# Kernel optimization log

Measured on AMD Instinct MI355X. Metric: run time of the kernel, lower is better.

## Reference

```python
import jax, jax.numpy as jnp
import numpy as np

N_NODES = 50000
N_EDGES = 800000
IN_CH = 128
OUT_CH = 32
HID = 2 * OUT_CH  # 64


def setup_inputs() -> dict:
    key = jax.random.key(0)
    ks = jax.random.split(key, 8)
    x = jax.random.normal(ks[0], (N_NODES, IN_CH), dtype=jnp.float32)
    edge_index = jax.random.randint(ks[1], (2, N_EDGES), 0, N_NODES, dtype=jnp.int32)
    s1 = 1.0 / np.sqrt(IN_CH)
    s2 = 1.0 / np.sqrt(HID)
    W1 = jax.random.normal(ks[2], (IN_CH, HID), dtype=jnp.float32) * s1
    b1 = jnp.zeros((HID,), dtype=jnp.float32)
    W_mu = jax.random.normal(ks[3], (HID, OUT_CH), dtype=jnp.float32) * s2
    b_mu = jnp.zeros((OUT_CH,), dtype=jnp.float32)
    W_logstd = jax.random.normal(ks[4], (HID, OUT_CH), dtype=jnp.float32) * s2
    b_logstd = jnp.zeros((OUT_CH,), dtype=jnp.float32)
    return {"x": x, "edge_index": edge_index, "W1": W1, "b1": b1,
            "W_mu": W_mu, "b_mu": b_mu, "W_logstd": W_logstd, "b_logstd": b_logstd}


def _gcn_norm(edge_index, n, dtype):
    # PyG GCNConv: add self-loops, symmetric normalization D^-1/2 A D^-1/2
    loops = jnp.arange(n, dtype=edge_index.dtype)
    src = jnp.concatenate([edge_index[0], loops])
    dst = jnp.concatenate([edge_index[1], loops])
    deg = jax.ops.segment_sum(jnp.ones_like(dst, dtype=dtype), dst, num_segments=n)
    deg_inv_sqrt = jnp.where(deg > 0, jax.lax.rsqrt(deg), 0.0)
    norm = deg_inv_sqrt[src] * deg_inv_sqrt[dst]  # [E+N]
    return src, dst, norm


def _gcn_conv(x, W, b, src, dst, norm, n):
    h = x @ W                        # transform first (in >= out)
    msg = h[src] * norm[:, None]     # gather + scale, [E+N, out]
    out = jax.ops.segment_sum(msg, dst, num_segments=n)
    return out + b


def reference(x, edge_index, W1, b1, W_mu, b_mu, W_logstd, b_logstd):
    n = x.shape[0]
    src, dst, norm = _gcn_norm(edge_index, n, x.dtype)
    h = jax.nn.relu(_gcn_conv(x, W1, b1, src, dst, norm, n))
    mu = _gcn_conv(h, W_mu, b_mu, src, dst, norm, n)
    logstd = _gcn_conv(h, W_logstd, b_logstd, src, dst, norm, n)
    return mu, logstd
```

## Files before the change

kernel.cpp:

```cpp
#include <hip/hip_runtime.h>
#include <hip/hip_fp16.h>

#define N_NODES 50000
#define N_EDGES 800000
#define IN_CH 128
#define HID 64
#define OUT_CH 32
#define CAP 64
#define ZROW N_NODES

union H4 { uint2 u; __half2 h[2]; };

__global__ __launch_bounds__(256) void k_scatter(const int* __restrict__ ei,
                                                 int* cur, int* __restrict__ pk,
                                                 unsigned* zA, unsigned* zB) {
    if (blockIdx.x == 0 && threadIdx.x < 32) { zA[threadIdx.x] = 0u; zB[threadIdx.x] = 0u; }
    int g = blockIdx.x * 256 + threadIdx.x;
    if (g >= N_EDGES / 2) return;
    int2 ss = ((const int2*)ei)[g];
    int2 dd = ((const int2*)(ei + N_EDGES))[g];
    int p0 = (dd.x << 6) + atomicAdd(&cur[dd.x], 1);
    pk[p0] = ss.x;
    int p1 = (dd.y << 6) + atomicAdd(&cur[dd.y], 1);
    pk[p1] = ss.y;
}

__global__ __launch_bounds__(256) void k_mm1(const float* __restrict__ x,
                                             const float* __restrict__ W1,
                                             const int* __restrict__ cur,
                                             __half* __restrict__ t1) {
    __shared__ float4 ws[64 * 16];
    __shared__ float  xsT[64 * 64];
    int t = threadIdx.x;
    int n0 = blockIdx.x * 64;
    int lane = t & 63, wv_ = t >> 6;
    int ni = lane >> 2;
    int cq = ((lane & 3) << 2) + wv_;
    const float4* W4 = (const float4*)W1;
    const float4* x4 = (const float4*)x;
    float4 acc0 = {0,0,0,0}, acc1 = acc0, acc2 = acc0, acc3 = acc0;
#pragma unroll
    for (int kt = 0; kt < 2; ++kt) {
        __syncthreads();
#pragma unroll
        for (int i = 0; i < 4; ++i) {
            int L = i * 256 + t;
            ws[L] = W4[kt * 1024 + L];
            int n = L >> 4, q = L & 15;
            int ng = n0 + n; if (ng >= N_NODES) ng = N_NODES - 1;
            float4 v = x4[ng * 32 + kt * 16 + q];
            int fb = q * 256 + (((n >> 2) ^ q) << 2) + (n & 3);
            xsT[fb]       = v.x;
            xsT[fb + 64]  = v.y;
            xsT[fb + 128] = v.z;
            xsT[fb + 192] = v.w;
        }
        __syncthreads();
        const float4* xsT4 = (const float4*)xsT;
#pragma unroll 8
        for (int k = 0; k < 64; ++k) {
            float4 xv = xsT4[k * 16 + (ni ^ (k >> 2))];
            float4 wvv = ws[k * 16 + cq];
            acc0.x += xv.x * wvv.x; acc0.y += xv.x * wvv.y; acc0.z += xv.x * wvv.z; acc0.w += xv.x * wvv.w;
            acc1.x += xv.y * wvv.x; acc1.y += xv.y * wvv.y; acc1.z += xv.y * wvv.z; acc1.w += xv.y * wvv.w;
            acc2.x += xv.z * wvv.x; acc2.y += xv.z * wvv.y; acc2.z += xv.z * wvv.z; acc2.w += xv.z * wvv.w;
            acc3.x += xv.w * wvv.x; acc3.y += xv.w * wvv.y; acc3.z += xv.w * wvv.z; acc3.w += xv.w * wvv.w;
        }
    }
    int nb = n0 + 4 * ni;
    if (nb < N_NODES) {
        int4 c4 = *(const int4*)(cur + nb);
        float d0 = rsqrtf((float)c4.x + 1.0f);
        float d1 = rsqrtf((float)c4.y + 1.0f);
        float d2 = rsqrtf((float)c4.z + 1.0f);
        float d3 = rsqrtf((float)c4.w + 1.0f);
        uint2* o2 = (uint2*)t1;
        H4 v;
        v.h[0] = __floats2half2_rn(d0 * acc0.x, d0 * acc0.y);
        v.h[1] = __floats2half2_rn(d0 * acc0.z, d0 * acc0.w);
        o2[(nb + 0) * 16 + cq] = v.u;
        v.h[0] = __floats2half2_rn(d1 * acc1.x, d1 * acc1.y);
        v.h[1] = __floats2half2_rn(d1 * acc1.z, d1 * acc1.w);
        o2[(nb + 1) * 16 + cq] = v.u;
        v.h[0] = __floats2half2_rn(d2 * acc2.x, d2 * acc2.y);
        v.h[1] = __floats2half2_rn(d2 * acc2.z, d2 * acc2.w);
        o2[(nb + 2) * 16 + cq] = v.u;
        v.h[0] = __floats2half2_rn(d3 * acc3.x, d3 * acc3.y);
        v.h[1] = __floats2half2_rn(d3 * acc3.z, d3 * acc3.w);
        o2[(nb + 3) * 16 + cq] = v.u;
    }
}

__global__ __launch_bounds__(256) void k_agg(const int* __restrict__ pk,
                                             const int* __restrict__ cur,
                                             const __half* __restrict__ in,
                                             const float* __restrict__ bias,
                                             __half* __restrict__ out,
                                             int apply_relu) {
    int w = (blockIdx.x * 256 + threadIdx.x) >> 6;
    if (w >= N_NODES) return;
    int lane = threadIdx.x & 63;
    int eg = lane >> 3, cs = lane & 7;
    int cnt = cur[w];
    int beg = w << 6, end = beg + cnt;
    const uint4* __restrict__ inv = (const uint4*)in;
    float acc[8] = {0,0,0,0,0,0,0,0};
#pragma unroll 2
    for (int base = beg; base < end; base += 8) {
        int je = base + eg;
        int s = (je < end) ? pk[je] : ZROW;
        uint4 r = inv[s * 8 + cs];
        const __half2* h2 = (const __half2*)&r;
        float2 f;
        f = __half22float2(h2[0]); acc[0] += f.x; acc[1] += f.y;
        f = __half22float2(h2[1]); acc[2] += f.x; acc[3] += f.y;
        f = __half22float2(h2[2]); acc[4] += f.x; acc[5] += f.y;
        f = __half22float2(h2[3]); acc[6] += f.x; acc[7] += f.y;
    }
#pragma unroll
    for (int m = 8; m <= 32; m <<= 1)
#pragma unroll
        for (int i = 0; i < 8; ++i) acc[i] += __shfl_xor(acc[i], m, 64);
    if (eg == 0) {
        uint4 sr = inv[w * 8 + cs];
        const __half2* sh = (const __half2*)&sr;
        float2 f;
        f = __half22float2(sh[0]); acc[0] += f.x; acc[1] += f.y;
        f = __half22float2(sh[1]); acc[2] += f.x; acc[3] += f.y;
        f = __half22float2(sh[2]); acc[4] += f.x; acc[5] += f.y;
        f = __half22float2(sh[3]); acc[6] += f.x; acc[7] += f.y;
        float dw = rsqrtf((float)cnt + 1.0f);
        if (apply_relu) {
            float4 b0 = ((const float4*)bias)[2 * cs];
            float4 b1v = ((const float4*)bias)[2 * cs + 1];
            acc[0] = dw * fmaxf(dw * acc[0] + b0.x, 0.f);
            acc[1] = dw * fmaxf(dw * acc[1] + b0.y, 0.f);
            acc[2] = dw * fmaxf(dw * acc[2] + b0.z, 0.f);
            acc[3] = dw * fmaxf(dw * acc[3] + b0.w, 0.f);
            acc[4] = dw * fmaxf(dw * acc[4] + b1v.x, 0.f);
            acc[5] = dw * fmaxf(dw * acc[5] + b1v.y, 0.f);
            acc[6] = dw * fmaxf(dw * acc[6] + b1v.z, 0.f);
            acc[7] = dw * fmaxf(dw * acc[7] + b1v.w, 0.f);
        } else {
#pragma unroll
            for (int i = 0; i < 8; ++i) acc[i] *= dw;
        }
        __half2 o[4];
        o[0] = __floats2half2_rn(acc[0], acc[1]);
        o[1] = __floats2half2_rn(acc[2], acc[3]);
        o[2] = __floats2half2_rn(acc[4], acc[5]);
        o[3] = __floats2half2_rn(acc[6], acc[7]);
        ((uint4*)out)[w * 8 + cs] = *(const uint4*)o;
    }
}

__global__ __launch_bounds__(256) void k_mm2(const __half* __restrict__ agg2,
                                             const float* __restrict__ Wmu,
                                             const float* __restrict__ bmu,
                                             const float* __restrict__ Wls,
                                             const float* __restrict__ bls,
                                             float* __restrict__ out) {
    __shared__ float4 ws[64 * 16];
    __shared__ float  xsT[64 * 64];
    int t = threadIdx.x;
    int n0 = blockIdx.x * 64;
    int lane = t & 63, wv_ = t >> 6;
    int ni = lane >> 2;
    int cq = ((lane & 3) << 2) + wv_;
    const float4* Wm4 = (const float4*)Wmu;
    const float4* Wl4 = (const float4*)Wls;
    const uint2*  x2  = (const uint2*)agg2;
#pragma unroll
    for (int i = 0; i < 4; ++i) {
        int L = i * 256 + t;
        int k = L >> 4, c = L & 15;
        ws[L] = (c < 8) ? Wm4[k * 8 + c] : Wl4[k * 8 + (c - 8)];
        int n = L >> 4, q = L & 15;
        int ng = n0 + n; if (ng >= N_NODES) ng = N_NODES - 1;
        H4 hv; hv.u = x2[ng * 16 + q];
        float2 f0 = __half22float2(hv.h[0]), f1 = __half22float2(hv.h[1]);
        int fb = q * 256 + (((n >> 2) ^ q) << 2) + (n & 3);
        xsT[fb]       = f0.x;
        xsT[fb + 64]  = f0.y;
        xsT[fb + 128] = f1.x;
        xsT[fb + 192] = f1.y;
    }
    float4 b = (cq < 8) ? ((const float4*)bmu)[cq] : ((const float4*)bls)[cq - 8];
    float4 acc0 = b, acc1 = b, acc2 = b, acc3 = b;
    __syncthreads();
    const float4* xsT4 = (const float4*)xsT;
#pragma unroll 8
    for (int k = 0; k < 64; ++k) {
        float4 xv = xsT4[k * 16 + (ni ^ (k >> 2))];
        float4 wvv = ws[k * 16 + cq];
        acc0.x += xv.x * wvv.x; acc0.y += xv.x * wvv.y; acc0.z += xv.x * wvv.z; acc0.w += xv.x * wvv.w;
        acc1.x += xv.y * wvv.x; acc1.y += xv.y * wvv.y; acc1.z += xv.y * wvv.z; acc1.w += xv.y * wvv.w;
        acc2.x += xv.z * wvv.x; acc2.y += xv.z * wvv.y; acc2.z += xv.z * wvv.z; acc2.w += xv.z * wvv.w;
        acc3.x += xv.w * wvv.x; acc3.y += xv.w * wvv.y; acc3.z += xv.w * wvv.z; acc3.w += xv.w * wvv.w;
    }
    int nb = n0 + 4 * ni;
    if (nb < N_NODES) {
        float4* o4 = (float4*)out;
        long base_off = (cq < 8) ? 0 : (long)N_NODES * 8;
        int cq8 = cq & 7;
        o4[base_off + (long)(nb + 0) * 8 + cq8] = acc0;
        o4[base_off + (long)(nb + 1) * 8 + cq8] = acc1;
        o4[base_off + (long)(nb + 2) * 8 + cq8] = acc2;
        o4[base_off + (long)(nb + 3) * 8 + cq8] = acc3;
    }
}

extern "C" void kernel_launch(void* const* d_in, const int* in_sizes, int n_in,
                              void* d_out, int out_size, void* d_ws, size_t ws_size,
                              hipStream_t stream) {
    const float* x   = (const float*)d_in[0];
    const int*   ei  = (const int*)  d_in[1];
    const float* W1  = (const float*)d_in[2];
    const float* b1  = (const float*)d_in[3];
    const float* Wmu = (const float*)d_in[4];
    const float* bmu = (const float*)d_in[5];
    const float* Wls = (const float*)d_in[6];
    const float* bls = (const float*)d_in[7];
    float* out = (float*)d_out;

    int*   cur  = (int*)d_ws;
    int*   pk   = (int*)d_ws + 50048;
    __half* bufA = (__half*)((int*)d_ws + 3250048);
    __half* bufB = (__half*)((int*)d_ws + 4850080);
    __half* bufC = (__half*)((int*)d_ws + 6450112);

    hipMemsetAsync(d_ws, 0, 200000, stream);
    k_scatter <<<1563, 256, 0, stream>>>(ei, cur, pk,
                   (unsigned*)(bufA + (size_t)ZROW * HID),
                   (unsigned*)(bufB + (size_t)ZROW * HID));
    k_mm1     <<<782, 256, 0, stream>>>(x, W1, cur, bufA);
    k_agg     <<<12500, 256, 0, stream>>>(pk, cur, bufA, b1, bufB, 1);
    k_agg     <<<12500, 256, 0, stream>>>(pk, cur, bufB, nullptr, bufC, 0);
    k_mm2     <<<782, 256, 0, stream>>>(bufC, Wmu, bmu, Wls, bls, out);
}
```

Baseline: 200.0 us.

## Use 16-bit neighbor indices, padded degree counters, and vectorized index loads

New measurement: 206.5 us. +3.3%, slower.

```diff
diff --git a/kernel.cpp b/kernel.cpp
--- a/kernel.cpp
+++ b/kernel.cpp
@@ -8,21 +8,22 @@
 #define OUT_CH 32
 #define CAP 64
 #define ZROW N_NODES
+#define CURS 16
 
 union H4 { uint2 u; __half2 h[2]; };
 
 __global__ __launch_bounds__(256) void k_scatter(const int* __restrict__ ei,
-                                                 int* cur, int* __restrict__ pk,
+                                                 int* cur, unsigned short* __restrict__ pk,
                                                  unsigned* zA, unsigned* zB) {
     if (blockIdx.x == 0 && threadIdx.x < 32) { zA[threadIdx.x] = 0u; zB[threadIdx.x] = 0u; }
     int g = blockIdx.x * 256 + threadIdx.x;
     if (g >= N_EDGES / 2) return;
     int2 ss = ((const int2*)ei)[g];
     int2 dd = ((const int2*)(ei + N_EDGES))[g];
-    int p0 = (dd.x << 6) + atomicAdd(&cur[dd.x], 1);
-    pk[p0] = ss.x;
-    int p1 = (dd.y << 6) + atomicAdd(&cur[dd.y], 1);
-    pk[p1] = ss.y;
+    int p0 = (dd.x << 6) + atomicAdd(&cur[dd.x << 4], 1);
+    pk[p0] = (unsigned short)ss.x;
+    int p1 = (dd.y << 6) + atomicAdd(&cur[dd.y << 4], 1);
+    pk[p1] = (unsigned short)ss.y;
 }
 
 __global__ __launch_bounds__(256) void k_mm1(const float* __restrict__ x,
@@ -69,11 +70,10 @@
     }
     int nb = n0 + 4 * ni;
     if (nb < N_NODES) {
-        int4 c4 = *(const int4*)(cur + nb);
-        float d0 = rsqrtf((float)c4.x + 1.0f);
-        float d1 = rsqrtf((float)c4.y + 1.0f);
-        float d2 = rsqrtf((float)c4.z + 1.0f);
-        float d3 = rsqrtf((float)c4.w + 1.0f);
+        float d0 = rsqrtf((float)cur[(nb + 0) << 4] + 1.0f);
+        float d1 = rsqrtf((float)cur[(nb + 1) << 4] + 1.0f);
+        float d2 = rsqrtf((float)cur[(nb + 2) << 4] + 1.0f);
+        float d3 = rsqrtf((float)cur[(nb + 3) << 4] + 1.0f);
         uint2* o2 = (uint2*)t1;
         H4 v;
         v.h[0] = __floats2half2_rn(d0 * acc0.x, d0 * acc0.y);
@@ -91,7 +91,7 @@
     }
 }
 
-__global__ __launch_bounds__(256) void k_agg(const int* __restrict__ pk,
+__global__ __launch_bounds__(256) void k_agg(const unsigned short* __restrict__ pk,
                                              const int* __restrict__ cur,
                                              const __half* __restrict__ in,
                                              const float* __restrict__ bias,
@@ -101,21 +101,23 @@
     if (w >= N_NODES) return;
     int lane = threadIdx.x & 63;
     int eg = lane >> 3, cs = lane & 7;
-    int cnt = cur[w];
-    int beg = w << 6, end = beg + cnt;
+    int cnt = __builtin_amdgcn_readfirstlane(cur[w << 4]);
     const uint4* __restrict__ inv = (const uint4*)in;
     float acc[8] = {0,0,0,0,0,0,0,0};
-#pragma unroll 2
-    for (int base = beg; base < end; base += 8) {
-        int je = base + eg;
-        int s = (je < end) ? pk[je] : ZROW;
-        uint4 r = inv[s * 8 + cs];
-        const __half2* h2 = (const __half2*)&r;
-        float2 f;
-        f = __half22float2(h2[0]); acc[0] += f.x; acc[1] += f.y;
-        f = __half22float2(h2[1]); acc[2] += f.x; acc[3] += f.y;
-        f = __half22float2(h2[2]); acc[4] += f.x; acc[5] += f.y;
-        f = __half22float2(h2[3]); acc[6] += f.x; acc[7] += f.y;
+    if (eg * 8 < cnt) {
+        uint4 p4 = ((const uint4*)pk)[w * 8 + eg];
+        const unsigned short* us = (const unsigned short*)&p4;
+#pragma unroll
+        for (int i = 0; i < 8; ++i) {
+            int s = (eg * 8 + i < cnt) ? (int)us[i] : ZROW;
+            uint4 r = inv[s * 8 + cs];
+            const __half2* h2 = (const __half2*)&r;
+            float2 f;
+            f = __half22float2(h2[0]); acc[0] += f.x; acc[1] += f.y;
+            f = __half22float2(h2[1]); acc[2] += f.x; acc[3] += f.y;
+            f = __half22float2(h2[2]); acc[4] += f.x; acc[5] += f.y;
+            f = __half22float2(h2[3]); acc[6] += f.x; acc[7] += f.y;
+        }
     }
 #pragma unroll
     for (int m = 8; m <= 32; m <<= 1)
@@ -224,12 +226,12 @@
     float* out = (float*)d_out;
 
     int*   cur  = (int*)d_ws;
-    int*   pk   = (int*)d_ws + 50048;
-    __half* bufA = (__half*)((int*)d_ws + 3250048);
-    __half* bufB = (__half*)((int*)d_ws + 4850080);
-    __half* bufC = (__half*)((int*)d_ws + 6450112);
-
-    hipMemsetAsync(d_ws, 0, 200000, stream);
+    unsigned short* pk = (unsigned short*)((int*)d_ws + 800000);
+    __half* bufA = (__half*)((int*)d_ws + 2400000);
+    __half* bufB = (__half*)((int*)d_ws + 4000064);
+    __half* bufC = (__half*)((int*)d_ws + 5600128);
+
+    hipMemsetAsync(d_ws, 0, 3200000, stream);
     k_scatter <<<1563, 256, 0, stream>>>(ei, cur, pk,
                    (unsigned*)(bufA + (size_t)ZROW * HID),
                    (unsigned*)(bufB + (size_t)ZROW * HID));
```

## Partition edge scatter by destination range and store neighbor indices as uint16

Applied to the files above, without the earlier changes.

Measured after the change: 196.3 us. About the same (-1.8%).

```diff
diff --git a/kernel.cpp b/kernel.cpp
--- a/kernel.cpp
+++ b/kernel.cpp
@@ -8,21 +8,34 @@
 #define OUT_CH 32
 #define CAP 64
 #define ZROW N_NODES
+#define PART_SZ 6250
 
 union H4 { uint2 u; __half2 h[2]; };
 
 __global__ __launch_bounds__(256) void k_scatter(const int* __restrict__ ei,
-                                                 int* cur, int* __restrict__ pk,
+                                                 int* cur, unsigned short* __restrict__ pk,
                                                  unsigned* zA, unsigned* zB) {
-    if (blockIdx.x == 0 && threadIdx.x < 32) { zA[threadIdx.x] = 0u; zB[threadIdx.x] = 0u; }
-    int g = blockIdx.x * 256 + threadIdx.x;
+    if (blockIdx.x == 0) {
+        int t = threadIdx.x;
+        if (t < 32) zA[t] = 0u;
+        else if (t < 64) zB[t - 32] = 0u;
+    }
+    int part = blockIdx.x & 7;
+    int g = (blockIdx.x >> 3) * 256 + threadIdx.x;
     if (g >= N_EDGES / 2) return;
+    int2 dd = ((const int2*)(ei + N_EDGES))[g];
+    bool a0 = (unsigned)(dd.x - part * PART_SZ) < (unsigned)PART_SZ;
+    bool a1 = (unsigned)(dd.y - part * PART_SZ) < (unsigned)PART_SZ;
+    if (!a0 && !a1) return;
     int2 ss = ((const int2*)ei)[g];
-    int2 dd = ((const int2*)(ei + N_EDGES))[g];
-    int p0 = (dd.x << 6) + atomicAdd(&cur[dd.x], 1);
-    pk[p0] = ss.x;
-    int p1 = (dd.y << 6) + atomicAdd(&cur[dd.y], 1);
-    pk[p1] = ss.y;
+    if (a0) {
+        int pos = (dd.x << 6) + atomicAdd(&cur[dd.x], 1);
+        pk[pos] = (unsigned short)ss.x;
+    }
+    if (a1) {
+        int pos = (dd.y << 6) + atomicAdd(&cur[dd.y], 1);
+        pk[pos] = (unsigned short)ss.y;
+    }
 }
 
 __global__ __launch_bounds__(256) void k_mm1(const float* __restrict__ x,
@@ -91,7 +104,7 @@
     }
 }
 
-__global__ __launch_bounds__(256) void k_agg(const int* __restrict__ pk,
+__global__ __launch_bounds__(256) void k_agg(const unsigned short* __restrict__ pk,
                                              const int* __restrict__ cur,
                                              const __half* __restrict__ in,
                                              const float* __restrict__ bias,
@@ -101,14 +114,14 @@
     if (w >= N_NODES) return;
     int lane = threadIdx.x & 63;
     int eg = lane >> 3, cs = lane & 7;
-    int cnt = cur[w];
+    int cnt = __builtin_amdgcn_readfirstlane(cur[w]);
     int beg = w << 6, end = beg + cnt;
     const uint4* __restrict__ inv = (const uint4*)in;
     float acc[8] = {0,0,0,0,0,0,0,0};
 #pragma unroll 2
     for (int base = beg; base < end; base += 8) {
         int je = base + eg;
-        int s = (je < end) ? pk[je] : ZROW;
+        int s = (je < end) ? (int)pk[je] : ZROW;
         uint4 r = inv[s * 8 + cs];
         const __half2* h2 = (const __half2*)&r;
         float2 f;
@@ -224,17 +237,17 @@
     float* out = (float*)d_out;
 
     int*   cur  = (int*)d_ws;
-    int*   pk   = (int*)d_ws + 50048;
-    __half* bufA = (__half*)((int*)d_ws + 3250048);
-    __half* bufB = (__half*)((int*)d_ws + 4850080);
-    __half* bufC = (__half*)((int*)d_ws + 6450112);
+    unsigned short* pk = (unsigned short*)((int*)d_ws + 50176);
+    __half* bufA = (__half*)((int*)d_ws + 1650176);
+    __half* bufB = (__half*)((int*)d_ws + 3250304);
+    __half* bufC = (__half*)((int*)d_ws + 4850432);
 
     hipMemsetAsync(d_ws, 0, 200000, stream);
-    k_scatter <<<1563, 256, 0, stream>>>(ei, cur, pk,
+    k_scatter <<<1563 * 8, 256, 0, stream>>>(ei, cur, pk,
                    (unsigned*)(bufA + (size_t)ZROW * HID),
                    (unsigned*)(bufB + (size_t)ZROW * HID));
-    k_mm1     <<<782, 256, 0, stream>>>(x, W1, cur, bufA);
-    k_agg     <<<12500, 256, 0, stream>>>(pk, cur, bufA, b1, bufB, 1);
-    k_agg     <<<12500, 256, 0, stream>>>(pk, cur, bufB, nullptr, bufC, 0);
-    k_mm2     <<<782, 256, 0, stream>>>(bufC, Wmu, bmu, Wls, bls, out);
-}
+    k_mm1 <<<782, 256, 0, stream>>>(x, W1, cur, bufA);
+    k_agg <<<12500, 256, 0, stream>>>(pk, cur, bufA, b1, bufB, 1);
+    k_agg <<<12500, 256, 0, stream>>>(pk, cur, bufB, nullptr, bufC, 0);
+    k_mm2 <<<782, 256, 0, stream>>>(bufC, Wmu, bmu, Wls, bls, out);
+}
```
